# Optimization experiments

Hardware: AMD Instinct MI355X
Metric: run time of the kernel (lower is better)

The kernel has to match this reference:

```python
import jax, jax.numpy as jnp
import numpy as np

N, E, G = 50000, 800000, 64
IN, HID, H1, H2, OUT = 128, 64, 4, 4, 10
NEG_SLOPE = 0.2


def gat_layer(h, src, dst, W, attn_l, attn_r, bias, n_nodes, n_heads, d):
    # h: [N, F_in] -> feat: [N, H, D]
    feat = (h @ W).reshape(n_nodes, n_heads, d)
    el = jnp.sum(feat * attn_l, axis=-1)          # [N, H]
    er = jnp.sum(feat * attn_r, axis=-1)          # [N, H]
    e = jax.nn.leaky_relu(el[src] + er[dst], NEG_SLOPE)  # [E, H]
    # edge softmax per destination node (numerically stable)
    m = jax.ops.segment_max(e, dst, num_segments=n_nodes)   # [N, H]
    ex = jnp.exp(e - m[dst])                                 # [E, H]
    s = jax.ops.segment_sum(ex, dst, num_segments=n_nodes)   # [N, H]
    alpha = ex / s[dst]                                      # [E, H]
    msg = alpha[:, :, None] * feat[src]                      # [E, H, D]
    out = jax.ops.segment_sum(msg, dst, num_segments=n_nodes)  # [N, H, D]
    return jax.nn.elu(out + bias.reshape(1, n_heads, d))


def setup_inputs() -> dict:
    key = jax.random.key(0)
    ks = jax.random.split(key, 16)
    x = jax.random.normal(ks[0], (N, IN), dtype=jnp.float32)
    src = jax.random.randint(ks[1], (E,), 0, N, dtype=jnp.int32)
    dst = jax.random.randint(ks[2], (E,), 0, N, dtype=jnp.int32)
    graph_ids = jnp.sort(jax.random.randint(ks[3], (N,), 0, G, dtype=jnp.int32))
    sc1 = 1.0 / np.sqrt(IN)
    sc2 = 1.0 / np.sqrt(HID * H1)
    W1 = jax.random.normal(ks[4], (IN, H1 * HID), dtype=jnp.float32) * sc1
    attn_l1 = jax.random.normal(ks[5], (H1, HID), dtype=jnp.float32) * 0.1
    attn_r1 = jax.random.normal(ks[6], (H1, HID), dtype=jnp.float32) * 0.1
    b1 = jnp.zeros((H1 * HID,), dtype=jnp.float32)
    W2 = jax.random.normal(ks[7], (H1 * HID, H2 * HID), dtype=jnp.float32) * sc2
    attn_l2 = jax.random.normal(ks[8], (H2, HID), dtype=jnp.float32) * 0.1
    attn_r2 = jax.random.normal(ks[9], (H2, HID), dtype=jnp.float32) * 0.1
    b2 = jnp.zeros((H2 * HID,), dtype=jnp.float32)
    fcW = jax.random.normal(ks[10], (HID, OUT), dtype=jnp.float32) * (1.0 / np.sqrt(HID))
    fcb = jnp.zeros((OUT,), dtype=jnp.float32)
    return {"x": x, "src": src, "dst": dst, "graph_ids": graph_ids,
            "W1": W1, "attn_l1": attn_l1, "attn_r1": attn_r1, "b1": b1,
            "W2": W2, "attn_l2": attn_l2, "attn_r2": attn_r2, "b2": b2,
            "fcW": fcW, "fcb": fcb}


def reference(x, src, dst, graph_ids, W1, attn_l1, attn_r1, b1,
              W2, attn_l2, attn_r2, b2, fcW, fcb):
    h = gat_layer(x, src, dst, W1, attn_l1, attn_r1, b1, N, H1, HID)
    h = h.reshape(N, H1 * HID)                    # flatten heads (layer 0)
    h = gat_layer(h, src, dst, W2, attn_l2, attn_r2, b2, N, H2, HID)
    h = h.mean(axis=1)                            # mean over heads (layer 1) -> [N, HID]
    pooled = jax.ops.segment_sum(h, graph_ids, num_segments=G)  # SumPooling -> [G, HID]
    return pooled @ fcW + fcb                     # dropout is identity in eval
```

## Files before the change

kernel.cpp:

```cpp
#include <hip/hip_runtime.h>
#include <math.h>

#define NN 50000
#define MPAD 50048
#define NE 800000
#define NG 64
#define FIN 128
#define FH 256
#define HID 64
#define NH 4
#define NOUT 10
#define NEG_SLOPE 0.2f
#define NSB ((NN + 1023) / 1024)

typedef unsigned short u16;
typedef __attribute__((ext_vector_type(8))) short short8;
typedef __attribute__((ext_vector_type(4))) float f32x4;

static __device__ __forceinline__ float leaky(float x){ return x > 0.f ? x : NEG_SLOPE * x; }
static __device__ __forceinline__ float elu1(float x){ return x > 0.f ? x : (__expf(x) - 1.f); }
static __device__ __forceinline__ float b2f(u16 u){
  union { unsigned int i; float f; } v; v.i = ((unsigned)u) << 16; return v.f;
}
static __device__ __forceinline__ u16 f2b(float f){
  union { float f; unsigned int i; } v; v.f = f;
  unsigned r = v.i + 0x7FFFu + ((v.i >> 16) & 1u);
  return (u16)(r >> 16);
}

static __device__ __forceinline__ void gl_lds16(const u16* g, u16* l){
  __builtin_amdgcn_global_load_lds(
      (const __attribute__((address_space(1))) void*)g,
      (__attribute__((address_space(3))) void*)l, 16, 0, 0);
}

#define HIST_BLKS ((NE + 255) / 256)
#define F2B_BLKS (NN * FIN / 4 / 256)
#define W1_BLKS  (FIN * FH / 256)
#define W2_BLKS  (FH * FH / 256)
__global__ void k_histprep(const int* __restrict__ dst, int* __restrict__ cnt,
                           int* __restrict__ rank,
                           const float* __restrict__ x, u16* __restrict__ xh,
                           const float* __restrict__ W1, u16* __restrict__ Wt1,
                           const float* __restrict__ W2, u16* __restrict__ Wt2,
                           float* __restrict__ pooled)
{
  int b = blockIdx.x;
  if (b < HIST_BLKS){
    int i = b * 256 + threadIdx.x;
    if (i < NE) rank[i] = atomicAdd(&cnt[dst[i]], 1);
  } else if (b < HIST_BLKS + F2B_BLKS){
    int i = ((b - HIST_BLKS) * 256 + threadIdx.x) * 4;
    float4 v = *reinterpret_cast<const float4*>(x + i);
    ushort4 o; o.x = f2b(v.x); o.y = f2b(v.y); o.z = f2b(v.z); o.w = f2b(v.w);
    *reinterpret_cast<ushort4*>(xh + i) = o;
  } else if (b < HIST_BLKS + F2B_BLKS + W1_BLKS){
    int e = (b - HIST_BLKS - F2B_BLKS) * 256 + threadIdx.x;
    int k = e >> 8, c = e & 255;
    Wt1[(size_t)c * FIN + k] = f2b(W1[e]);
  } else if (b < HIST_BLKS + F2B_BLKS + W1_BLKS + W2_BLKS){
    int e = (b - HIST_BLKS - F2B_BLKS - W1_BLKS) * 256 + threadIdx.x;
    int k = e >> 8, c = e & 255;
    Wt2[(size_t)c * FH + k] = f2b(W2[e]);
  } else {
    float4 z = make_float4(0.f, 0.f, 0.f, 0.f);
    #pragma unroll
    for (int l = 0; l < 4; l++)
      *reinterpret_cast<float4*>(pooled + (l * 256 + threadIdx.x) * 4) = z;
  }
}

__global__ __launch_bounds__(256) void k_scan1(const int* __restrict__ cnt,
    int* __restrict__ offs, int* __restrict__ bsum)
{
  __shared__ int wsum[4];
  int t = threadIdx.x;
  int lane = t & 63, wv = t >> 6;
  int base = blockIdx.x * 1024 + t * 4;
  int4 v = make_int4(0, 0, 0, 0);
  if (base + 3 < NN) v = *reinterpret_cast<const int4*>(cnt + base);
  else {
    if (base + 0 < NN) v.x = cnt[base + 0];
    if (base + 1 < NN) v.y = cnt[base + 1];
    if (base + 2 < NN) v.z = cnt[base + 2];
  }
  int s = v.x + v.y + v.z + v.w;
  int incl = s;
  #pragma unroll
  for (int d = 1; d < 64; d <<= 1){
    int u = __shfl_up(incl, d);
    if (lane >= d) incl += u;
  }
  if (lane == 63) wsum[wv] = incl;
  __syncthreads();
  int woff = 0;
  #pragma unroll
  for (int i = 0; i < 4; i++) if (i < wv) woff += wsum[i];
  int texcl = woff + incl - s;
  int e0 = texcl, e1 = e0 + v.x, e2 = e1 + v.y, e3 = e2 + v.z;
  if (base + 3 < NN) *reinterpret_cast<int4*>(offs + base) = make_int4(e0, e1, e2, e3);
  else {
    if (base + 0 < NN) offs[base + 0] = e0;
    if (base + 1 < NN) offs[base + 1] = e1;
    if (base + 2 < NN) offs[base + 2] = e2;
  }
  if (t == 255) bsum[blockIdx.x] = woff + incl;
}

static __device__ __forceinline__ void block_bpre(const int* __restrict__ bsum,
                                                  int* sb)
{
  int t = threadIdx.x;
  if (t < 64){
    int s = (t < NSB) ? bsum[t] : 0;
    int incl = s;
    #pragma unroll
    for (int d = 1; d < 64; d <<= 1){
      int u = __shfl_up(incl, d);
      if (t >= d) incl += u;
    }
    sb[t] = incl - s;
  }
  __syncthreads();
}

__global__ __launch_bounds__(256) void k_scatter(const int* __restrict__ src,
    const int* __restrict__ dst, const int* __restrict__ offs,
    const int* __restrict__ bsum, const int* __restrict__ rank,
    int* __restrict__ csrc){
  __shared__ int sb[64];
  block_bpre(bsum, sb);
  int i = blockIdx.x * blockDim.x + threadIdx.x;
  if (i < NE){
    int d = dst[i];
    csrc[offs[d] + sb[d >> 10] + rank[i]] = src[i];
  }
}

template<int K>
__global__ __launch_bounds__(512) void k_gemm_bf(
    const u16* __restrict__ A, const u16* __restrict__ Wt, u16* __restrict__ C,
    const float* __restrict__ attn_l, const float* __restrict__ attn_r,
    float* __restrict__ el, float* __restrict__ er)
{
  __shared__ union {
    struct { u16 a[128 * 32]; u16 b[256 * 32]; } s;
    u16 ct[128 * 256];
  } L;
  int t = threadIdx.x;
  int wv = t >> 6, lane = t & 63;
  int row0 = blockIdx.x * 128;
  int lr = lane & 15, lk = lane >> 4;
  int wm = wv >> 2, wn = wv & 3;

  f32x4 acc[4][4];
  #pragma unroll
  for (int m = 0; m < 4; m++)
    #pragma unroll
    for (int n = 0; n < 4; n++) acc[m][n] = (f32x4){0.f, 0.f, 0.f, 0.f};

  const u16* asrc = A + (size_t)(row0 + wv * 16 + (lane >> 2)) * K + (lane & 3) * 8;
  u16* aldst = &L.s.a[wv * 512];
  const u16* bsrc0 = Wt + (size_t)(wv * 32 + (lane >> 2)) * K + (lane & 3) * 8;
  const u16* bsrc1 = Wt + (size_t)(wv * 32 + 16 + (lane >> 2)) * K + (lane & 3) * 8;
  u16* bldst0 = &L.s.b[wv * 1024];
  u16* bldst1 = &L.s.b[wv * 1024 + 512];

  for (int k0 = 0; k0 < K; k0 += 32){
    gl_lds16(asrc + k0, aldst);
    gl_lds16(bsrc0 + k0, bldst0);
    gl_lds16(bsrc1 + k0, bldst1);
    __syncthreads();
    short8 af[4], bf[4];
    #pragma unroll
    for (int m = 0; m < 4; m++)
      af[m] = *reinterpret_cast<const short8*>(&L.s.a[(wm * 64 + m * 16 + lr) * 32 + lk * 8]);
    #pragma unroll
    for (int n = 0; n < 4; n++)
      bf[n] = *reinterpret_cast<const short8*>(&L.s.b[(wn * 64 + n * 16 + lr) * 32 + lk * 8]);
    #pragma unroll
    for (int m = 0; m < 4; m++)
      #pragma unroll
      for (int n = 0; n < 4; n++)
        acc[m][n] = __builtin_amdgcn_mfma_f32_16x16x32_bf16(af[m], bf[n], acc[m][n], 0, 0, 0);
    __syncthreads();
  }

  int rg = lane >> 4;
  #pragma unroll
  for (int m = 0; m < 4; m++)
    #pragma unroll
    for (int n = 0; n < 4; n++)
      #pragma unroll
      for (int r = 0; r < 4; r++)
        L.ct[(wm * 64 + m * 16 + rg * 4 + r) * 256 + wn * 64 + n * 16 + lr] = f2b(acc[m][n][r]);
  __syncthreads();
  #pragma unroll
  for (int l = 0; l < 8; l++){
    int idx = t + l * 512;
    int row = idx >> 5, colg = idx & 31;
    short8 v = *reinterpret_cast<const short8*>(&L.ct[row * 256 + colg * 8]);
    *reinterpret_cast<short8*>(C + (size_t)(row0 + row) * 256 + colg * 8) = v;
  }

  {
    int r = t >> 2, hh = t & 3;
    const u16* crow = &L.ct[r * 256 + hh * 64];
    float pl = 0.f, pr = 0.f;
    #pragma unroll
    for (int d8 = 0; d8 < 8; d8++){
      short8 cv = *reinterpret_cast<const short8*>(crow + d8 * 8);
      const float* alp = &attn_l[hh * 64 + d8 * 8];
      const float* arp = &attn_r[hh * 64 + d8 * 8];
      #pragma unroll
      for (int q = 0; q < 8; q++){
        float fv = b2f((u16)cv[q]);
        pl = fmaf(fv, alp[q], pl);
        pr = fmaf(fv, arp[q], pr);
      }
    }
    int orow = row0 + r;
    el[orow * 4 + hh] = pl;
    er[orow * 4 + hh] = pr;
  }
}

template<int LAYER>
__global__ __launch_bounds__(256) void k_agg2(const u16* __restrict__ feat,
    const float* __restrict__ el, const float* __restrict__ er,
    const int* __restrict__ offs, const int* __restrict__ bsum,
    const int* __restrict__ cnt, const int* __restrict__ csrc,
    const float* __restrict__ bias, void* __restrict__ outv)
{
  __shared__ int sb[64];
  block_bpre(bsum, sb);
  int wv = threadIdx.x >> 6, lane = threadIdx.x & 63;
  int n = blockIdx.x * 4 + wv;
  int e0 = offs[n] + sb[n >> 10];
  int deg = cnt[n];
  int hs = lane & 3, slot = lane >> 2;
  int half = lane >> 5, k = lane & 31;
  int hk = k >> 3;
  float erh = er[n * 4 + hs];

  float srun_l = 0.f;
  float a[8];
  #pragma unroll
  for (int p = 0; p < 8; p++) a[p] = 0.f;

  for (int base = 0; base < deg; base += 16){
    int cntc = min(16, deg - base);
    int idx = base + slot;
    int sj = 0; float ex = 0.f;
    if (idx < deg){
      sj = csrc[e0 + idx];
      ex = __expf(leaky(el[sj * 4 + hs] + erh));
    }
    srun_l += ex;
    int jjmax = (cntc + 1) >> 1;
    for (int jj = 0; jj < jjmax; jj++){
      int e = jj * 2 + half;
      float w = __shfl(ex, e * 4 + hk);
      int sjj = __shfl(sj, e * 4);
      short8 fv = *reinterpret_cast<const short8*>(feat + (size_t)sjj * FH + k * 8);
      #pragma unroll
      for (int p = 0; p < 8; p++) a[p] = fmaf(w, b2f((u16)fv[p]), a[p]);
    }
  }

  #pragma unroll
  for (int d = 4; d < 64; d <<= 1) srun_l += __shfl_xor(srun_l, d);
  float invh = (deg > 0) ? 1.f / srun_l : 0.f;
  float inv = __shfl(invh, hk);
  #pragma unroll
  for (int p = 0; p < 8; p++) a[p] += __shfl_xor(a[p], 32);

  float4 bv0 = *reinterpret_cast<const float4*>(&bias[k * 8]);
  float4 bv1 = *reinterpret_cast<const float4*>(&bias[k * 8 + 4]);
  float ev[8];
  ev[0] = elu1(a[0] * inv + bv0.x); ev[1] = elu1(a[1] * inv + bv0.y);
  ev[2] = elu1(a[2] * inv + bv0.z); ev[3] = elu1(a[3] * inv + bv0.w);
  ev[4] = elu1(a[4] * inv + bv1.x); ev[5] = elu1(a[5] * inv + bv1.y);
  ev[6] = elu1(a[6] * inv + bv1.z); ev[7] = elu1(a[7] * inv + bv1.w);

  if (LAYER == 1){
    if (lane < 32){
      u16* out = (u16*)outv;
      short8 o;
      #pragma unroll
      for (int p = 0; p < 8; p++) o[p] = (short)f2b(ev[p]);
      *reinterpret_cast<short8*>(out + (size_t)n * FH + k * 8) = o;
    }
  } else {
    #pragma unroll
    for (int p = 0; p < 8; p++){
      ev[p] += __shfl_xor(ev[p], 8);
      ev[p] += __shfl_xor(ev[p], 16);
      ev[p] *= 0.25f;
    }
    if (lane < 8){
      float* out = (float*)outv;
      float4 o0 = make_float4(ev[0], ev[1], ev[2], ev[3]);
      float4 o1 = make_float4(ev[4], ev[5], ev[6], ev[7]);
      *reinterpret_cast<float4*>(out + (size_t)n * HID + lane * 8) = o0;
      *reinterpret_cast<float4*>(out + (size_t)n * HID + lane * 8 + 4) = o1;
    }
  }
}

__global__ __launch_bounds__(256) void k_pool(const float* __restrict__ h2,
    const int* __restrict__ gid, float* __restrict__ pooled)
{
  int wv = threadIdx.x >> 6, lane = threadIdx.x & 63;
  int w = blockIdx.x * 4 + wv;
  int base = w * 64;
  if (base >= NN) return;
  int grp = lane >> 4, c4 = (lane & 15) * 4;
  int curg = -1;
  float4 acc = make_float4(0.f, 0.f, 0.f, 0.f);
  #pragma unroll 4
  for (int it = 0; it < 16; it++){
    int row = base + it * 4 + grp;
    if (row >= NN) break;
    int g = gid[row];
    if (g != curg){
      if (curg >= 0){
        atomicAdd(&pooled[curg * HID + c4 + 0], acc.x);
        atomicAdd(&pooled[curg * HID + c4 + 1], acc.y);
        atomicAdd(&pooled[curg * HID + c4 + 2], acc.z);
        atomicAdd(&pooled[curg * HID + c4 + 3], acc.w);
      }
      curg = g; acc = make_float4(0.f, 0.f, 0.f, 0.f);
    }
    float4 v = *reinterpret_cast<const float4*>(&h2[(size_t)row * HID + c4]);
    acc.x += v.x; acc.y += v.y; acc.z += v.z; acc.w += v.w;
  }
  if (curg >= 0){
    atomicAdd(&pooled[curg * HID + c4 + 0], acc.x);
    atomicAdd(&pooled[curg * HID + c4 + 1], acc.y);
    atomicAdd(&pooled[curg * HID + c4 + 2], acc.z);
    atomicAdd(&pooled[curg * HID + c4 + 3], acc.w);
  }
}

__global__ void k_fc(const float* __restrict__ pooled, const float* __restrict__ fcW,
                     const float* __restrict__ fcb, float* __restrict__ out)
{
  int t = threadIdx.x;
  if (t >= NG * NOUT) return;
  int g = t / NOUT, o = t % NOUT;
  float s = fcb[o];
  for (int d = 0; d < HID; d++) s = fmaf(pooled[g * HID + d], fcW[d * NOUT + o], s);
  out[t] = s;
}

static inline size_t align_up(size_t x){ return (x + 255) & ~(size_t)255; }

extern "C" void kernel_launch(void* const* d_in, const int* in_sizes, int n_in,
                              void* d_out, int out_size, void* d_ws, size_t ws_size,
                              hipStream_t stream) {
  const float* x    = (const float*)d_in[0];
  const int*   src  = (const int*)d_in[1];
  const int*   dst  = (const int*)d_in[2];
  const int*   gid  = (const int*)d_in[3];
  const float* W1   = (const float*)d_in[4];
  const float* al1  = (const float*)d_in[5];
  const float* ar1  = (const float*)d_in[6];
  const float* b1   = (const float*)d_in[7];
  const float* W2   = (const float*)d_in[8];
  const float* al2  = (const float*)d_in[9];
  const float* ar2  = (const float*)d_in[10];
  const float* b2   = (const float*)d_in[11];
  const float* fcW  = (const float*)d_in[12];
  const float* fcb  = (const float*)d_in[13];
  float* out = (float*)d_out;

  char* p = (char*)d_ws;
  int* cnt  = (int*)p; p += align_up((size_t)NN * 4);
  int* offs = (int*)p; p += align_up((size_t)NN * 4);
  int* bsum = (int*)p; p += align_up((size_t)NSB * 4);
  int* rank = (int*)p; p += align_up((size_t)NE * 4);
  int* csrc = (int*)p; p += align_up((size_t)NE * 4);
  u16* xh    = (u16*)p; p += align_up((size_t)MPAD * FIN * 2);
  u16* feath = (u16*)p; p += align_up((size_t)MPAD * FH * 2);
  u16* h1h   = (u16*)p; p += align_up((size_t)MPAD * FH * 2);
  float* elb = (float*)p; p += align_up((size_t)MPAD * NH * 4);
  float* erb = (float*)p; p += align_up((size_t)MPAD * NH * 4);
  float* h2  = (float*)p; p += align_up((size_t)NN * HID * 4);
  float* pooled = (float*)p; p += align_up((size_t)NG * HID * 4);
  u16* Wt1 = (u16*)p; p += align_up((size_t)FIN * FH * 2);
  u16* Wt2 = (u16*)p; p += align_up((size_t)FH * FH * 2);

  hipMemsetAsync(cnt, 0, (size_t)NN * 4, stream);

  const int EB = (NE + 255) / 256;
  const int NB4 = (NN + 3) / 4;
  const int GB = MPAD / 128;
  const int HP = HIST_BLKS + F2B_BLKS + W1_BLKS + W2_BLKS + 1;

  k_histprep<<<HP, 256, 0, stream>>>(dst, cnt, rank, x, xh, W1, Wt1, W2, Wt2, pooled);
  k_scan1<<<NSB, 256, 0, stream>>>(cnt, offs, bsum);
  k_scatter<<<EB, 256, 0, stream>>>(src, dst, offs, bsum, rank, csrc);

  k_gemm_bf<FIN><<<GB, 512, 0, stream>>>(xh, Wt1, feath, al1, ar1, elb, erb);
  k_agg2<1><<<NB4, 256, 0, stream>>>(feath, elb, erb, offs, bsum, cnt, csrc, b1, h1h);

  k_gemm_bf<FH><<<GB, 512, 0, stream>>>(h1h, Wt2, feath, al2, ar2, elb, erb);
  k_agg2<2><<<NB4, 256, 0, stream>>>(feath, elb, erb, offs, bsum, cnt, csrc, b2, h2);

  k_pool<<<(NN + 255) / 256, 256, 0, stream>>>(h2, gid, pooled);
  k_fc<<<1, 640, 0, stream>>>(pooled, fcW, fcb, out);
}
```

Before: 270.5 us.

## Reorder layer-1 GAT as aggregate-then-project with precomputed attention vectors

Layer 1 now folds the attention vectors into W1, so el/er come from a 128-wide dot product on x. It then aggregates raw bf16 x rows (128-wide) per head before a GEMM that applies W1 per head, bias and ELU. The gather now reads 128-wide rows instead of 256-wide projected features, and the separate projection GEMM before aggregation is gone. In exchange it writes and reads a 4x128 per-node intermediate and the GEMM tile grows, and el/er are computed from bf16 x instead of bf16 projected features, which slightly changes numerics.

```diff
diff --git a/kernel.cpp b/kernel.cpp
--- a/kernel.cpp
+++ b/kernel.cpp
@@ -38,11 +38,14 @@
 #define F2B_BLKS (NN * FIN / 4 / 256)
 #define W1_BLKS  (FIN * FH / 256)
 #define W2_BLKS  (FH * FH / 256)
+#define PW (HIST_BLKS + F2B_BLKS + W1_BLKS + W2_BLKS)
 __global__ void k_histprep(const int* __restrict__ dst, int* __restrict__ cnt,
                            int* __restrict__ rank,
                            const float* __restrict__ x, u16* __restrict__ xh,
                            const float* __restrict__ W1, u16* __restrict__ Wt1,
                            const float* __restrict__ W2, u16* __restrict__ Wt2,
+                           const float* __restrict__ al1, const float* __restrict__ ar1,
+                           float* __restrict__ wl1, float* __restrict__ wr1,
                            float* __restrict__ pooled)
 {
   int b = blockIdx.x;
@@ -58,15 +61,27 @@
     int e = (b - HIST_BLKS - F2B_BLKS) * 256 + threadIdx.x;
     int k = e >> 8, c = e & 255;
     Wt1[(size_t)c * FIN + k] = f2b(W1[e]);
-  } else if (b < HIST_BLKS + F2B_BLKS + W1_BLKS + W2_BLKS){
+  } else if (b < PW){
     int e = (b - HIST_BLKS - F2B_BLKS - W1_BLKS) * 256 + threadIdx.x;
     int k = e >> 8, c = e & 255;
     Wt2[(size_t)c * FH + k] = f2b(W2[e]);
-  } else {
+  } else if (b == PW){
     float4 z = make_float4(0.f, 0.f, 0.f, 0.f);
     #pragma unroll
     for (int l = 0; l < 4; l++)
       *reinterpret_cast<float4*>(pooled + (l * 256 + threadIdx.x) * 4) = z;
+  } else {
+    int t = threadIdx.x;
+    int row = t & 127;
+    const float* av = (t >> 7) ? ar1 : al1;
+    float* dstw = (t >> 7) ? wr1 : wl1;
+    const float* Wr = W1 + (size_t)row * 256;
+    float s[4] = {0.f, 0.f, 0.f, 0.f};
+    #pragma unroll
+    for (int h = 0; h < 4; h++)
+      for (int d = 0; d < 64; d++)
+        s[h] = fmaf(Wr[h * 64 + d], av[h * 64 + d], s[h]);
+    *reinterpret_cast<float4*>(dstw + row * 4) = make_float4(s[0], s[1], s[2], s[3]);
   }
 }
 
@@ -137,6 +152,183 @@
   }
 }
 
+__global__ __launch_bounds__(256) void k_el1(const u16* __restrict__ xh,
+    const float* __restrict__ wl1, const float* __restrict__ wr1,
+    float* __restrict__ el, float* __restrict__ er)
+{
+  int n = blockIdx.x * 256 + threadIdx.x;
+  if (n >= NN) return;
+  const u16* xr = xh + (size_t)n * FIN;
+  float e0 = 0.f, e1 = 0.f, e2 = 0.f, e3 = 0.f;
+  float r0 = 0.f, r1 = 0.f, r2 = 0.f, r3 = 0.f;
+  #pragma unroll
+  for (int d8 = 0; d8 < 16; d8++){
+    short8 xv = *reinterpret_cast<const short8*>(xr + d8 * 8);
+    #pragma unroll
+    for (int q = 0; q < 8; q++){
+      float xf = b2f((u16)xv[q]);
+      int d = d8 * 8 + q;
+      float4 wl = *reinterpret_cast<const float4*>(wl1 + d * 4);
+      float4 wr = *reinterpret_cast<const float4*>(wr1 + d * 4);
+      e0 = fmaf(xf, wl.x, e0); e1 = fmaf(xf, wl.y, e1);
+      e2 = fmaf(xf, wl.z, e2); e3 = fmaf(xf, wl.w, e3);
+      r0 = fmaf(xf, wr.x, r0); r1 = fmaf(xf, wr.y, r1);
+      r2 = fmaf(xf, wr.z, r2); r3 = fmaf(xf, wr.w, r3);
+    }
+  }
+  *reinterpret_cast<float4*>(el + n * 4) = make_float4(e0, e1, e2, e3);
+  *reinterpret_cast<float4*>(er + n * 4) = make_float4(r0, r1, r2, r3);
+}
+
+__global__ __launch_bounds__(256) void k_agg1(const u16* __restrict__ xh,
+    const float* __restrict__ el, const float* __restrict__ er,
+    const int* __restrict__ offs, const int* __restrict__ bsum,
+    const int* __restrict__ cnt, const int* __restrict__ csrc,
+    u16* __restrict__ xa)
+{
+  __shared__ int sb[64];
+  block_bpre(bsum, sb);
+  int wv = threadIdx.x >> 6, lane = threadIdx.x & 63;
+  int n = blockIdx.x * 4 + wv;
+  int e0 = offs[n] + sb[n >> 10];
+  int deg = cnt[n];
+  int hs = lane & 3, slot = lane >> 2;
+  int q4 = lane >> 4, k = lane & 15;
+  float erh = er[n * 4 + hs];
+
+  float srun_l = 0.f;
+  float a0[8], a1[8], a2[8], a3[8];
+  #pragma unroll
+  for (int p = 0; p < 8; p++){ a0[p] = 0.f; a1[p] = 0.f; a2[p] = 0.f; a3[p] = 0.f; }
+
+  for (int base = 0; base < deg; base += 16){
+    int cntc = min(16, deg - base);
+    int idx = base + slot;
+    int sj = 0; float ex = 0.f;
+    if (idx < deg){
+      sj = csrc[e0 + idx];
+      ex = __expf(leaky(el[sj * 4 + hs] + erh));
+    }
+    srun_l += ex;
+    int jjmax = (cntc + 3) >> 2;
+    for (int jj = 0; jj < jjmax; jj++){
+      int e = jj * 4 + q4;
+      int sje = __shfl(sj, e * 4);
+      float w0 = __shfl(ex, e * 4 + 0);
+      float w1 = __shfl(ex, e * 4 + 1);
+      float w2 = __shfl(ex, e * 4 + 2);
+      float w3 = __shfl(ex, e * 4 + 3);
+      short8 fv = *reinterpret_cast<const short8*>(xh + (size_t)sje * FIN + k * 8);
+      #pragma unroll
+      for (int p = 0; p < 8; p++){
+        float xf = b2f((u16)fv[p]);
+        a0[p] = fmaf(w0, xf, a0[p]);
+        a1[p] = fmaf(w1, xf, a1[p]);
+        a2[p] = fmaf(w2, xf, a2[p]);
+        a3[p] = fmaf(w3, xf, a3[p]);
+      }
+    }
+  }
+
+  #pragma unroll
+  for (int d = 4; d < 64; d <<= 1) srun_l += __shfl_xor(srun_l, d);
+  float invh = (deg > 0) ? 1.f / srun_l : 0.f;
+  float i0 = __shfl(invh, 0), i1 = __shfl(invh, 1);
+  float i2 = __shfl(invh, 2), i3 = __shfl(invh, 3);
+  #pragma unroll
+  for (int p = 0; p < 8; p++){
+    a0[p] += __shfl_xor(a0[p], 16); a0[p] += __shfl_xor(a0[p], 32);
+    a1[p] += __shfl_xor(a1[p], 16); a1[p] += __shfl_xor(a1[p], 32);
+    a2[p] += __shfl_xor(a2[p], 16); a2[p] += __shfl_xor(a2[p], 32);
+    a3[p] += __shfl_xor(a3[p], 16); a3[p] += __shfl_xor(a3[p], 32);
+  }
+  if (lane < 16){
+    short8 o0, o1, o2, o3;
+    #pragma unroll
+    for (int p = 0; p < 8; p++){
+      o0[p] = (short)f2b(a0[p] * i0);
+      o1[p] = (short)f2b(a1[p] * i1);
+      o2[p] = (short)f2b(a2[p] * i2);
+      o3[p] = (short)f2b(a3[p] * i3);
+    }
+    u16* base0 = xa + ((size_t)n * NH) * FIN + k * 8;
+    *reinterpret_cast<short8*>(base0 + 0 * FIN) = o0;
+    *reinterpret_cast<short8*>(base0 + 1 * FIN) = o1;
+    *reinterpret_cast<short8*>(base0 + 2 * FIN) = o2;
+    *reinterpret_cast<short8*>(base0 + 3 * FIN) = o3;
+  }
+}
+
+__global__ __launch_bounds__(512) void k_gemm1(
+    const u16* __restrict__ xa, const u16* __restrict__ Wt1,
+    const float* __restrict__ b1, u16* __restrict__ C)
+{
+  __shared__ union {
+    struct { u16 a[4 * 128 * 32]; u16 b[256 * 32]; } s;
+    u16 ct[128 * 256];
+  } L;
+  int t = threadIdx.x;
+  int wv = t >> 6, lane = t & 63;
+  int row0 = blockIdx.x * 128;
+  int lr = lane & 15, lk = lane >> 4;
+  int wm = wv >> 2, wn = wv & 3;
+
+  f32x4 acc[4][4];
+  #pragma unroll
+  for (int m = 0; m < 4; m++)
+    #pragma unroll
+    for (int n = 0; n < 4; n++) acc[m][n] = (f32x4){0.f, 0.f, 0.f, 0.f};
+
+  const u16* asrcb = xa + (size_t)(row0 + wv * 16 + (lane >> 2)) * (NH * FIN) + (lane & 3) * 8;
+  const u16* bsrc0 = Wt1 + (size_t)(wv * 32 + (lane >> 2)) * FIN + (lane & 3) * 8;
+  const u16* bsrc1 = Wt1 + (size_t)(wv * 32 + 16 + (lane >> 2)) * FIN + (lane & 3) * 8;
+  u16* bldst0 = &L.s.b[wv * 1024];
+  u16* bldst1 = &L.s.b[wv * 1024 + 512];
+
+  for (int k0 = 0; k0 < FIN; k0 += 32){
+    #pragma unroll
+    for (int h = 0; h < 4; h++)
+      gl_lds16(asrcb + h * FIN + k0, &L.s.a[h * 4096 + wv * 512]);
+    gl_lds16(bsrc0 + k0, bldst0);
+    gl_lds16(bsrc1 + k0, bldst1);
+    __syncthreads();
+    short8 af[4], bf[4];
+    #pragma unroll
+    for (int m = 0; m < 4; m++)
+      af[m] = *reinterpret_cast<const short8*>(&L.s.a[wn * 4096 + (wm * 64 + m * 16 + lr) * 32 + lk * 8]);
+    #pragma unroll
+    for (int n = 0; n < 4; n++)
+      bf[n] = *reinterpret_cast<const short8*>(&L.s.b[(wn * 64 + n * 16 + lr) * 32 + lk * 8]);
+    #pragma unroll
+    for (int m = 0; m < 4; m++)
+      #pragma unroll
+      for (int n = 0; n < 4; n++)
+        acc[m][n] = __builtin_amdgcn_mfma_f32_16x16x32_bf16(af[m], bf[n], acc[m][n], 0, 0, 0);
+    __syncthreads();
+  }
+
+  float bcol[4];
+  #pragma unroll
+  for (int n = 0; n < 4; n++) bcol[n] = b1[wn * 64 + n * 16 + lr];
+  int rg = lane >> 4;
+  #pragma unroll
+  for (int m = 0; m < 4; m++)
+    #pragma unroll
+    for (int n = 0; n < 4; n++)
+      #pragma unroll
+      for (int r = 0; r < 4; r++)
+        L.ct[(wm * 64 + m * 16 + rg * 4 + r) * 256 + wn * 64 + n * 16 + lr] =
+            f2b(elu1(acc[m][n][r] + bcol[n]));
+  __syncthreads();
+  #pragma unroll
+  for (int l = 0; l < 8; l++){
+    int idx = t + l * 512;
+    int row = idx >> 5, colg = idx & 31;
+    short8 v = *reinterpret_cast<const short8*>(&L.ct[row * 256 + colg * 8]);
+    *reinterpret_cast<short8*>(C + (size_t)(row0 + row) * 256 + colg * 8) = v;
+  }
+}
+
 template<int K>
 __global__ __launch_bounds__(512) void k_gemm_bf(
     const u16* __restrict__ A, const u16* __restrict__ Wt, u16* __restrict__ C,
@@ -225,12 +417,11 @@
   }
 }
 
-template<int LAYER>
 __global__ __launch_bounds__(256) void k_agg2(const u16* __restrict__ feat,
     const float* __restrict__ el, const float* __restrict__ er,
     const int* __restrict__ offs, const int* __restrict__ bsum,
     const int* __restrict__ cnt, const int* __restrict__ csrc,
-    const float* __restrict__ bias, void* __restrict__ outv)
+    const float* __restrict__ bias, float* __restrict__ out)
 {
   __shared__ int sb[64];
   block_bpre(bsum, sb);
@@ -283,28 +474,17 @@
   ev[4] = elu1(a[4] * inv + bv1.x); ev[5] = elu1(a[5] * inv + bv1.y);
   ev[6] = elu1(a[6] * inv + bv1.z); ev[7] = elu1(a[7] * inv + bv1.w);
 
-  if (LAYER == 1){
-    if (lane < 32){
-      u16* out = (u16*)outv;
-      short8 o;
-      #pragma unroll
-      for (int p = 0; p < 8; p++) o[p] = (short)f2b(ev[p]);
-      *reinterpret_cast<short8*>(out + (size_t)n * FH + k * 8) = o;
-    }
-  } else {
-    #pragma unroll
-    for (int p = 0; p < 8; p++){
-      ev[p] += __shfl_xor(ev[p], 8);
-      ev[p] += __shfl_xor(ev[p], 16);
-      ev[p] *= 0.25f;
-    }
-    if (lane < 8){
-      float* out = (float*)outv;
-      float4 o0 = make_float4(ev[0], ev[1], ev[2], ev[3]);
-      float4 o1 = make_float4(ev[4], ev[5], ev[6], ev[7]);
-      *reinterpret_cast<float4*>(out + (size_t)n * HID + lane * 8) = o0;
-      *reinterpret_cast<float4*>(out + (size_t)n * HID + lane * 8 + 4) = o1;
-    }
+  #pragma unroll
+  for (int p = 0; p < 8; p++){
+    ev[p] += __shfl_xor(ev[p], 8);
+    ev[p] += __shfl_xor(ev[p], 16);
+    ev[p] *= 0.25f;
+  }
+  if (lane < 8){
+    float4 o0 = make_float4(ev[0], ev[1], ev[2], ev[3]);
+    float4 o1 = make_float4(ev[4], ev[5], ev[6], ev[7]);
+    *reinterpret_cast<float4*>(out + (size_t)n * HID + lane * 8) = o0;
+    *reinterpret_cast<float4*>(out + (size_t)n * HID + lane * 8 + 4) = o1;
   }
 }
 
@@ -382,6 +562,7 @@
   int* rank = (int*)p; p += align_up((size_t)NE * 4);
   int* csrc = (int*)p; p += align_up((size_t)NE * 4);
   u16* xh    = (u16*)p; p += align_up((size_t)MPAD * FIN * 2);
+  u16* xa    = (u16*)p; p += align_up((size_t)MPAD * NH * FIN * 2);
   u16* feath = (u16*)p; p += align_up((size_t)MPAD * FH * 2);
   u16* h1h   = (u16*)p; p += align_up((size_t)MPAD * FH * 2);
   float* elb = (float*)p; p += align_up((size_t)MPAD * NH * 4);
@@ -390,23 +571,28 @@
   float* pooled = (float*)p; p += align_up((size_t)NG * HID * 4);
   u16* Wt1 = (u16*)p; p += align_up((size_t)FIN * FH * 2);
   u16* Wt2 = (u16*)p; p += align_up((size_t)FH * FH * 2);
+  float* wl1 = (float*)p; p += align_up((size_t)FIN * NH * 4);
+  float* wr1 = (float*)p; p += align_up((size_t)FIN * NH * 4);
 
   hipMemsetAsync(cnt, 0, (size_t)NN * 4, stream);
 
   const int EB = (NE + 255) / 256;
   const int NB4 = (NN + 3) / 4;
   const int GB = MPAD / 128;
-  const int HP = HIST_BLKS + F2B_BLKS + W1_BLKS + W2_BLKS + 1;
-
-  k_histprep<<<HP, 256, 0, stream>>>(dst, cnt, rank, x, xh, W1, Wt1, W2, Wt2, pooled);
+  const int NEL = (NN + 255) / 256;
+  const int HP = PW + 2;
+
+  k_histprep<<<HP, 256, 0, stream>>>(dst, cnt, rank, x, xh, W1, Wt1, W2, Wt2,
+                                     al1, ar1, wl1, wr1, pooled);
   k_scan1<<<NSB, 256, 0, stream>>>(cnt, offs, bsum);
   k_scatter<<<EB, 256, 0, stream>>>(src, dst, offs, bsum, rank, csrc);
-
-  k_gemm_bf<FIN><<<GB, 512, 0, stream>>>(xh, Wt1, feath, al1, ar1, elb, erb);
-  k_agg2<1><<<NB4, 256, 0, stream>>>(feath, elb, erb, offs, bsum, cnt, csrc, b1, h1h);
+  k_el1<<<NEL, 256, 0, stream>>>(xh, wl1, wr1, elb, erb);
+
+  k_agg1<<<NB4, 256, 0, stream>>>(xh, elb, erb, offs, bsum, cnt, csrc, xa);
+  k_gemm1<<<GB, 512, 0, stream>>>(xa, Wt1, b1, h1h);
 
   k_gemm_bf<FH><<<GB, 512, 0, stream>>>(h1h, Wt2, feath, al2, ar2, elb, erb);
-  k_agg2<2><<<NB4, 256, 0, stream>>>(feath, elb, erb, offs, bsum, cnt, csrc, b2, h2);
+  k_agg2<<<NB4, 256, 0, stream>>>(feath, elb, erb, offs, bsum, cnt, csrc, b2, h2);
 
   k_pool<<<(NN + 255) / 256, 256, 0, stream>>>(h2, gid, pooled);
   k_fc<<<1, 640, 0, stream>>>(pooled, fcW, fcb, out);
```

Result: slower. 286.3 us (+5.8%).
